# Optimization experiments

Hardware: AMD Instinct MI355X
Metric: run time of the kernel (lower is better)

Reference implementation:

```python
import jax, jax.numpy as jnp
import numpy as np

D = 256       # vec_dim
HEADS = 8     # head_num
PS = 4        # patch_size
WS = 7        # window_size (in patches)
P = WS * WS   # tokens per window


def _relative_index():
    # replicates the torch meshgrid / relative coord logic (indexing='ij')
    coords = np.stack(np.meshgrid(np.arange(WS), np.arange(WS), indexing='ij'))  # [2,WS,WS]
    cf = coords.reshape(2, -1)                                                   # [2,P]
    rc = (cf[:, :, None] - cf[:, None, :]).transpose(1, 2, 0)                    # [P,P,2]
    rc[:, :, 0] += WS - 1
    rc[:, :, 1] += WS - 1
    rc[:, :, 1] *= 2 * WS - 1
    return rc.sum(-1)  # [P,P] ints in [0,(2WS-1)^2)


def _shift_mask(ch, cw):
    # standard swin shift mask built on the patch grid (ch, cw)
    fm = np.zeros((ch, cw))
    idx = (slice(0, -WS), slice(-WS, -(WS // 2)), slice(-(WS // 2), None))
    cnt = 0
    for y in idx:
        for x in idx:
            fm[y, x] = cnt
            cnt += 1
    nh, nw = ch // WS, cw // WS
    fm = fm.reshape(nh, WS, nw, WS).transpose(0, 2, 1, 3).reshape(nh * nw, P)
    m = fm[:, None, :] - fm[:, :, None]
    return np.where(m != 0, -100.0, 0.0).astype(np.float32)


def setup_inputs() -> dict:
    key = jax.random.key(0)
    ks = jax.random.split(key, 10)
    N, PN = 8, 3136
    s = 0.02
    return {
        'inputs': jax.random.normal(ks[0], (N, D, PN), jnp.float32),
        'Wk': jax.random.normal(ks[1], (HEADS * D, D), jnp.float32) * s,
        'bk': jax.random.normal(ks[2], (HEADS * D,), jnp.float32) * s,
        'Wq': jax.random.normal(ks[3], (HEADS * D, D), jnp.float32) * s,
        'bq': jax.random.normal(ks[4], (HEADS * D,), jnp.float32) * s,
        'Wv': jax.random.normal(ks[5], (HEADS * D, D), jnp.float32) * s,
        'bv': jax.random.normal(ks[6], (HEADS * D,), jnp.float32) * s,
        'Wo': jax.random.normal(ks[7], (D, HEADS * D), jnp.float32) * s,
        'bo': jax.random.normal(ks[8], (D,), jnp.float32) * s,
        'rel_code': jax.random.normal(ks[9], ((2 * WS - 1) ** 2, HEADS), jnp.float32) * 0.02,
        'h': 224,
        'w': 224,
    }


def _forward(inputs, Wk, bk, Wq, bq, Wv, bv, Wo, bo, rel_code, h, w):
    ch, cw = h // PS, w // PS            # patch grid
    N, _, PN = inputs.shape
    C = D // (PS * PS)
    nh, nw = ch // WS, cw // WS
    WIN = nh * nw

    # patches2features -> pixel-space roll by WS//2 -> features2patches
    x = inputs.reshape(N, C, PS, PS, ch, cw)
    x = x.transpose(0, 1, 4, 2, 5, 3).reshape(N, C, ch * PS, cw * PS)
    x = jnp.roll(x, (WS // 2, WS // 2), axis=(-2, -1))
    x = x.reshape(N, C, ch, PS, cw, PS).transpose(0, 2, 4, 1, 3, 5).reshape(N, PN, D)
    x = x.transpose(0, 2, 1)  # [N,D,PN]

    def proj(W, b):
        e = jnp.einsum('od,ndp->nop', W, x) + b[None, :, None]  # [N,HEADS*D,PN]
        e = e.reshape(N, HEADS, D, ch, cw)
        # window partition: n h d (nh w1)(nw w2) -> n h (nh nw) d (w1 w2)
        e = e.reshape(N, HEADS, D, nh, WS, nw, WS)
        return e.transpose(0, 1, 3, 5, 2, 4, 6).reshape(N, HEADS, WIN, D, P)

    k = proj(Wk, bk)
    q = proj(Wq, bq)
    v = proj(Wv, bv)

    # attn[p,q] = k_p . q_q  (softmax over keys p, axis=3)
    attn = jnp.einsum('nhgdp,nhgdq->nhgpq', k, q) / (D ** 0.5)
    mask = jnp.asarray(_shift_mask(ch, cw))
    attn = attn + mask[None, None]
    rel_idx = _relative_index().ravel()
    rel = rel_code[rel_idx].reshape(P, P, HEADS).transpose(2, 0, 1)  # [H,P,P]
    attn = attn + rel[None, :, None]
    wmap = jax.nn.softmax(attn, axis=3)

    out = jnp.einsum('nhgdp,nhgpq->nhgdq', v, wmap)
    # window merge back to [N,H,D,PN]
    out = out.reshape(N, HEADS, nh, nw, D, WS, WS)
    out = out.transpose(0, 1, 4, 2, 5, 3, 6).reshape(N, HEADS * D, PN)
    return jnp.einsum('od,ndp->nop', Wo, out) + bo[None, :, None]  # [N,D,PN]


def reference(inputs, Wk, bk, Wq, bq, Wv, bv, Wo, bo, rel_code, h, w):
    return _forward(inputs, Wk, bk, Wq, bq, Wv, bv, Wo, bo, rel_code, h, w)
```

## Files before the change

kernel.cpp:

```cpp
#include <hip/hip_runtime.h>
#include <hip/hip_bf16.h>


#define NBATCH 8
#define MSTR   2176
#define TROWS  3200

typedef unsigned short ushort_t;
typedef __attribute__((ext_vector_type(8))) short bf16x8;
typedef __attribute__((ext_vector_type(8))) unsigned short u16x8;
typedef __attribute__((ext_vector_type(4))) float f32x4;

__device__ __forceinline__ float b2f(ushort_t u) {
  union { unsigned int i; float f; } v; v.i = ((unsigned int)u) << 16; return v.f;
}
__device__ __forceinline__ ushort_t f2b(float f) {
  union { float f; unsigned int u; } v; v.f = f;
  unsigned int u = v.u;
  return (ushort_t)((u + 0x7FFFu + ((u >> 16) & 1u)) >> 16);
}
__device__ __forceinline__ int regof(int y) { return (y < 49) ? 0 : ((y < 53) ? 1 : 2); }
__device__ __forceinline__ int div7(int t) { return (t * 37) >> 8; }
__device__ __forceinline__ int tmap(int p, int gi, int gj) {
  int wi = div7(p); return (gi * 7 + wi) * 56 + gj * 7 + (p - wi * 7);
}
__device__ __forceinline__ ushort4 pack4(f32x4 a) {
  ushort4 u; u.x = f2b(a[0]); u.y = f2b(a[1]); u.z = f2b(a[2]); u.w = f2b(a[3]);
  return u;
}
__device__ __forceinline__ void gload_lds16(const ushort_t* g, ushort_t* l) {
  __builtin_amdgcn_global_load_lds(
      (const __attribute__((address_space(1))) void*)g,
      (__attribute__((address_space(3))) void*)l, 16, 0, 0);
}
__device__ __forceinline__ void sb0() { __builtin_amdgcn_sched_barrier(0); }

__global__ void k_prep(const float* __restrict__ Wk, const float* __restrict__ Wq,
                       const float* __restrict__ Wo, const float* __restrict__ Wv,
                       const float* __restrict__ bk, const float* __restrict__ bq,
                       const float* __restrict__ bv, const float* __restrict__ bo,
                       const float* __restrict__ relc,
                       ushort_t* __restrict__ Aext, ushort_t* __restrict__ Wov3,
                       float* __restrict__ cvec, float* __restrict__ relL2) {
  __shared__ float red[8];
  int blk = blockIdx.x, t = threadIdx.x;
  if (blk < 512) {
    int h = blk >> 6, b0 = (blk & 63) << 2, a = t;
    const float* wkh = Wk + h * 65536;
    const float* wqh = Wq + h * 65536;
    float a0 = 0.f, a1 = 0.f, a2 = 0.f, a3 = 0.f;
    for (int dd = 0; dd < 256; ++dd) {
      float wk = wkh[dd * 256 + a];
      float4 w4 = *(const float4*)(wqh + dd * 256 + b0);
      a0 += wk * w4.x; a1 += wk * w4.y; a2 += wk * w4.z; a3 += wk * w4.w;
    }
    ushort4 u; u.x = f2b(a0); u.y = f2b(a1); u.z = f2b(a2); u.w = f2b(a3);
    *(ushort4*)(Aext + (h * 256 + a) * 256 + b0) = u;
  } else if (blk < 1024) {
    int bb = blk - 512;
    int h = bb >> 6, o0 = (bb & 63) << 2, d = t;
    float a0 = 0.f, a1 = 0.f, a2 = 0.f, a3 = 0.f;
    for (int dd = 0; dd < 256; ++dd) {
      float wv = Wv[(h * 256 + dd) * 256 + d];
      a0 += Wo[(o0 + 0) * 2048 + h * 256 + dd] * wv;
      a1 += Wo[(o0 + 1) * 2048 + h * 256 + dd] * wv;
      a2 += Wo[(o0 + 2) * 2048 + h * 256 + dd] * wv;
      a3 += Wo[(o0 + 3) * 2048 + h * 256 + dd] * wv;
    }
    Wov3[(o0 + 0) * 2048 + h * 256 + d] = f2b(a0);
    Wov3[(o0 + 1) * 2048 + h * 256 + d] = f2b(a1);
    Wov3[(o0 + 2) * 2048 + h * 256 + d] = f2b(a2);
    Wov3[(o0 + 3) * 2048 + h * 256 + d] = f2b(a3);
  } else if (blk < 1032) {
    int h = blk - 1024;
    float s1 = 0.f, s2 = 0.f;
    for (int dd = 0; dd < 256; ++dd) {
      s1 += bk[h * 256 + dd] * Wq[(h * 256 + dd) * 256 + t];
      s2 += bq[h * 256 + dd] * Wk[(h * 256 + dd) * 256 + t];
    }
    Aext[(2048 + h) * 256 + t] = f2b(s1);
    Aext[(2056 + h) * 256 + t] = f2b(s2);
  } else if (blk == 1032) {
    for (int i = t; i < 112 * 256 / 8; i += 256)
      *(u16x8*)(Aext + 2064 * 256 + i * 8) = (u16x8){0,0,0,0,0,0,0,0};
  } else if (blk < 1289) {
    int o = blk - 1033;
    const float* wob = Wo + o * 2048;
    float acc = 0.f;
#pragma unroll
    for (int j = 0; j < 8; ++j) acc += wob[j * 256 + t] * bv[j * 256 + t];
#pragma unroll
    for (int s = 1; s < 64; s <<= 1) acc += __shfl_xor(acc, s);
    if ((t & 63) == 0) red[t >> 6] = acc;
    __syncthreads();
    if (t == 0) cvec[o] = bo[o] + red[0] + red[1] + red[2] + red[3];
  } else {
    if (t < 8) {
      float c = 0.f;
      for (int dd = 0; dd < 256; ++dd) c += bk[t * 256 + dd] * bq[t * 256 + dd];
      red[t] = c * 0.0625f;
    }
    __syncthreads();
    for (int i = t; i < 8 * 169; i += 256) {
      int h = i / 169, idx = i - h * 169;
      relL2[i] = relc[idx * 8 + h] + red[h];
    }
  }
}

__global__ void k_conv(const float* __restrict__ X, ushort_t* __restrict__ Xroll) {
  const int n = blockIdx.x / 57, y = blockIdx.x % 57;
  ushort_t* xr = Xroll + (size_t)n * TROWS * 256;
  const int d = threadIdx.x;
  if (y == 56) {
    for (int i = d; i < 64 * 256 / 8; i += 256)
      *(u16x8*)(xr + 3136 * 256 + i * 8) = (u16x8){0,0,0,0,0,0,0,0};
    return;
  }
  const int c = d >> 4, p1 = (d >> 2) & 3, p2 = d & 3;
  const int sp = c * 16 + (((p1 + 1) & 3) << 2) + ((p2 + 1) & 3);
  const int ty = (p1 == 3) ? y : ((y == 0) ? 55 : y - 1);
  const float* rowp = X + (size_t)n * 256 * 3136 + sp * 3136 + ty * 56;
  ushort_t* orow = xr + y * 56 * 256 + d;
  for (int x = 0; x < 56; ++x) {
    int tx = (p2 == 3) ? x : ((x == 0) ? 55 : x - 1);
    orow[x * 256] = f2b(rowp[tx]);
  }
}

__global__ __launch_bounds__(256, 2) void k_gemm1(
    const ushort_t* __restrict__ Xroll, const ushort_t* __restrict__ Aext,
    ushort_t* __restrict__ MT) {
  const int bx0 = blockIdx.x;
  const int n = bx0 & 7;
  const int inner = bx0 >> 3;
  const int aa = inner % 17;
  const int c  = inner / 17;
  const int a0 = aa * 128;
  const int tstart = (c == 0) ? 0 : (7 * c + 1);
  const int T = (c == 0) ? 8 : 7;
  const int tid = threadIdx.x, wave = tid >> 6, lane = tid & 63;
  const int quad = lane >> 4, l16 = lane & 15;
  const int wa = wave >> 1, wt = wave & 1;
  const ushort_t* Xn = Xroll + (size_t)n * TROWS * 256;
  ushort_t* Mn = MT + (size_t)n * TROWS * MSTR;

  const ushort_t* abase = Aext + (size_t)(a0 + wa * 64 + l16) * 256 + quad * 8;
  bf16x8 areg[8][4];
#pragma unroll
  for (int kk = 0; kk < 8; ++kk)
#pragma unroll
    for (int i = 0; i < 4; ++i)
      areg[kk][i] = *(const bf16x8*)(abase + i * 4096 + kk * 32);
  sb0();

  const ushort_t* bbase =
      Xn + (size_t)(tstart * 64 + wt * 32 + l16) * 256 + quad * 8;

  for (int m = 0; m < T; ++m) {
    const ushort_t* bsrc = bbase + (size_t)m * 64 * 256;
    bf16x8 breg[8][2];
#pragma unroll
    for (int kk = 0; kk < 8; ++kk)
#pragma unroll
      for (int j = 0; j < 2; ++j)
        breg[kk][j] = *(const bf16x8*)(bsrc + j * 16 * 256 + kk * 32);
    sb0();

    f32x4 acc[4][2];
#pragma unroll
    for (int i = 0; i < 4; ++i)
#pragma unroll
      for (int j = 0; j < 2; ++j) acc[i][j] = (f32x4){0.f, 0.f, 0.f, 0.f};
#pragma unroll
    for (int kk = 0; kk < 8; ++kk)
#pragma unroll
      for (int i = 0; i < 4; ++i)
#pragma unroll
        for (int j = 0; j < 2; ++j)
          acc[i][j] = __builtin_amdgcn_mfma_f32_16x16x32_bf16(areg[kk][i], breg[kk][j], acc[i][j], 0, 0, 0);

    const int tb = (tstart + m) * 64;
#pragma unroll
    for (int i = 0; i < 4; ++i)
#pragma unroll
      for (int j = 0; j < 2; ++j) {
        int tg = tb + wt * 32 + j * 16 + l16;
        int ag = a0 + wa * 64 + i * 16 + quad * 4;
        *(ushort4*)(Mn + (size_t)tg * MSTR + ag) = pack4(acc[i][j]);
      }
  }
}

#define XP_STR 264
__global__ __launch_bounds__(512, 4) void k_attn2(
    const ushort_t* __restrict__ Xroll, ushort_t* __restrict__ MT,
    const float* __restrict__ relL2) {
  __shared__ ushort_t Xp[64 * XP_STR];
  __shared__ ushort_t StB[2][64 * 72];
  __shared__ float aqsL[8 * 64];
  __shared__ float bpsL[8 * 64];
  __shared__ float relLh[8 * 169];

  const int tid = threadIdx.x;
  const int wave = tid >> 6, lane = tid & 63;
  const int quad = lane >> 4, l16 = lane & 15;
  const int group = wave >> 2, wv = wave & 3;
  const int n = blockIdx.x >> 6, g = blockIdx.x & 63;
  const int gi = g >> 3, gj = g & 7;
  const ushort_t* Xn = Xroll + (size_t)n * TROWS * 256;
  ushort_t* Mn = MT + (size_t)n * TROWS * MSTR;

  {
    const int p = tid & 63, cg = tid >> 6;
    if (p < 49) {
      int t = tmap(p, gi, gj);
#pragma unroll
      for (int i = 0; i < 4; ++i)
        *(u16x8*)(&Xp[p * XP_STR + (cg * 4 + i) * 8]) =
            *(const u16x8*)(Xn + t * 256 + (cg * 4 + i) * 8);
    } else {
#pragma unroll
      for (int i = 0; i < 4; ++i)
        *(u16x8*)(&Xp[p * XP_STR + (cg * 4 + i) * 8]) = (u16x8){0,0,0,0,0,0,0,0};
    }
  }
  for (int i = tid; i < 8 * 169; i += 512) relLh[i] = relL2[i];
  {
    const int h = tid >> 6, q = tid & 63;
    int qq = (q < 49) ? q : 48;
    int t = tmap(qq, gi, gj);
    aqsL[h * 64 + q] = b2f(Mn[(size_t)t * MSTR + 2048 + h]);
    bpsL[h * 64 + q] = b2f(Mn[(size_t)t * MSTR + 2056 + h]);
  }
  __syncthreads();

  bf16x8 xfr[4][2];
#pragma unroll
  for (int dt = 0; dt < 4; ++dt) {
    const int d = (wv * 4 + dt) * 16 + l16;
#pragma unroll
    for (int kk = 0; kk < 2; ++kk)
#pragma unroll
      for (int j = 0; j < 8; ++j)
        xfr[dt][kk][j] = (short)Xp[(kk * 32 + quad * 8 + j) * XP_STR + d];
  }

  const int q = wv * 16 + l16;
  const int qq = (q < 49) ? q : 48;
  const int tq = tmap(qq, gi, gj);
  const ushort_t* Mbase = Mn + (size_t)tq * MSTR + quad * 8;
  const int yq = div7(qq), xq = qq - yq * 7;
  const int fq = regof(gi * 7 + yq) * 3 + regof(gj * 7 + xq);

  for (int hh = 0; hh < 4; ++hh) {
    const int h = hh * 2 + group;
    f32x4 sacc[4];
#pragma unroll
    for (int pt = 0; pt < 4; ++pt) sacc[pt] = (f32x4){0.f, 0.f, 0.f, 0.f};
    const ushort_t* mrow = Mbase + h * 256;
#pragma unroll
    for (int kk = 0; kk < 8; ++kk) {
      bf16x8 bfm = *(const bf16x8*)(mrow + kk * 32);
#pragma unroll
      for (int pt = 0; pt < 4; ++pt) {
        bf16x8 af = *(const bf16x8*)(&Xp[(pt * 16 + l16) * XP_STR + kk * 32 + quad * 8]);
        sacc[pt] = __builtin_amdgcn_mfma_f32_16x16x32_bf16(af, bfm, sacc[pt], 0, 0, 0);
      }
    }
    float v[16];
    const float aqv = aqsL[h * 64 + q];
    const float* rel_h = &relLh[h * 169];
    float m = -1e30f;
#pragma unroll
    for (int pt = 0; pt < 4; ++pt)
#pragma unroll
      for (int r = 0; r < 4; ++r) {
        int p = pt * 16 + quad * 4 + r;
        float val = -1e30f;
        if (p < 49) {
          int yp = div7(p), xp = p - yp * 7;
          int fp = regof(gi * 7 + yp) * 3 + regof(gj * 7 + xp);
          val = (sacc[pt][r] + aqv + bpsL[h * 64 + p]) * 0.0625f +
                rel_h[(yp - yq + 6) + 13 * (xp - xq + 6)];
          if (fp != fq) val -= 100.f;
        }
        v[pt * 4 + r] = val;
        m = fmaxf(m, val);
      }
    m = fmaxf(m, __shfl_xor(m, 16));
    m = fmaxf(m, __shfl_xor(m, 32));
    float s = 0.f;
#pragma unroll
    for (int i = 0; i < 16; ++i) { v[i] = __expf(v[i] - m); s += v[i]; }
    s += __shfl_xor(s, 16);
    s += __shfl_xor(s, 32);
    const float inv = 1.f / s;
    __syncthreads();
    {
      ushort_t* sb = &StB[group][q * 72];
#pragma unroll
      for (int pt = 0; pt < 4; ++pt) {
        ushort4 u;
        u.x = f2b(v[pt * 4 + 0] * inv); u.y = f2b(v[pt * 4 + 1] * inv);
        u.z = f2b(v[pt * 4 + 2] * inv); u.w = f2b(v[pt * 4 + 3] * inv);
        *(ushort4*)(&sb[pt * 16 + quad * 4]) = u;
      }
    }
    __syncthreads();
#pragma unroll
    for (int qt = 0; qt < 4; ++qt) {
      f32x4 tacc[4];
#pragma unroll
      for (int dt = 0; dt < 4; ++dt) tacc[dt] = (f32x4){0.f, 0.f, 0.f, 0.f};
#pragma unroll
      for (int kk = 0; kk < 2; ++kk) {
        bf16x8 bfw = *(const bf16x8*)(&StB[group][(qt * 16 + l16) * 72 + kk * 32 + quad * 8]);
#pragma unroll
        for (int dt = 0; dt < 4; ++dt)
          tacc[dt] = __builtin_amdgcn_mfma_f32_16x16x32_bf16(xfr[dt][kk], bfw, tacc[dt], 0, 0, 0);
      }
      int q2 = qt * 16 + l16;
      if (q2 < 49) {
        int t2 = tmap(q2, gi, gj);
#pragma unroll
        for (int dt = 0; dt < 4; ++dt) {
          int d0 = (wv * 4 + dt) * 16 + quad * 4;
          *(ushort4*)(Mn + (size_t)t2 * MSTR + h * 256 + d0) = pack4(tacc[dt]);
        }
      }
    }
  }
}

__global__ __launch_bounds__(256, 2) void k_gemm3(
    const ushort_t* __restrict__ Wov3, const ushort_t* __restrict__ MT,
    const float* __restrict__ cvec, float* __restrict__ out) {
  __shared__ ushort_t Asm[128 * 128];
  __shared__ ushort_t Bsm[128 * 128];
  const int bx0 = blockIdx.x;
  const int bx = (bx0 & 7) * 50 + (bx0 >> 3);
  const int n = bx / 50, r2 = bx % 50;
  const int oi = r2 / 25, tt = r2 % 25;
  const int o0 = oi * 128, t0 = tt * 128;
  const int tid = threadIdx.x, wave = tid >> 6, lane = tid & 63;
  const int quad = lane >> 4, l16 = lane & 15;
  const int wa = wave >> 1, wt = wave & 1;
  const ushort_t* Tn = MT + (size_t)n * TROWS * MSTR;
  float* on = out + (size_t)n * 256 * 3136;
  const int sw = l16 & 7;

  f32x4 acc[4][4];
#pragma unroll
  for (int i = 0; i < 4; ++i)
#pragma unroll
    for (int j = 0; j < 4; ++j) acc[i][j] = (f32x4){0.f, 0.f, 0.f, 0.f};

  for (int kit = 0; kit < 16; ++kit) {
    const int kb = kit * 128;
#pragma unroll
    for (int i = 0; i < 8; ++i) {
      int S = i * 256 + tid;
      int rr = S >> 4, sc = S & 15;
      int c = (sc & 8) | ((sc ^ rr) & 7);
      gload_lds16(Wov3 + (o0 + rr) * 2048 + kb + c * 8,
                  &Asm[(i * 256 + wave * 64) * 8]);
    }
#pragma unroll
    for (int i = 0; i < 8; ++i) {
      int S = i * 256 + tid;
      int rr = S >> 4, sc = S & 15;
      int c = (sc & 8) | ((sc ^ rr) & 7);
      gload_lds16(Tn + (size_t)(t0 + rr) * MSTR + kb + c * 8,
                  &Bsm[(i * 256 + wave * 64) * 8]);
    }
    __syncthreads();
#pragma unroll
    for (int kk = 0; kk < 4; ++kk) {
      bf16x8 af[4], bf[4];
      const int c = kk * 4 + quad;
      const int pos = (c & 8) | ((c ^ sw) & 7);
#pragma unroll
      for (int i = 0; i < 4; ++i)
        af[i] = *(const bf16x8*)(&Asm[(wa * 64 + i * 16 + l16) * 128 + pos * 8]);
#pragma unroll
      for (int j = 0; j < 4; ++j)
        bf[j] = *(const bf16x8*)(&Bsm[(wt * 64 + j * 16 + l16) * 128 + pos * 8]);
#pragma unroll
      for (int i = 0; i < 4; ++i)
#pragma unroll
        for (int j = 0; j < 4; ++j)
          acc[i][j] = __builtin_amdgcn_mfma_f32_16x16x32_bf16(af[i], bf[j], acc[i][j], 0, 0, 0);
    }
    __syncthreads();
  }
#pragma unroll
  for (int i = 0; i < 4; ++i) {
    const int ob = o0 + wa * 64 + i * 16 + quad * 4;
    const float4 cv = *(const float4*)(cvec + ob);
#pragma unroll
    for (int j = 0; j < 4; ++j) {
      const int tg = t0 + wt * 64 + j * 16 + l16;
      if (tg < 3136) {
        on[(size_t)(ob + 0) * 3136 + tg] = acc[i][j][0] + cv.x;
        on[(size_t)(ob + 1) * 3136 + tg] = acc[i][j][1] + cv.y;
        on[(size_t)(ob + 2) * 3136 + tg] = acc[i][j][2] + cv.z;
        on[(size_t)(ob + 3) * 3136 + tg] = acc[i][j][3] + cv.w;
      }
    }
  }
}

extern "C" void kernel_launch(void* const* d_in, const int* in_sizes, int n_in,
                              void* d_out, int out_size, void* d_ws, size_t ws_size,
                              hipStream_t stream) {
  (void)in_sizes; (void)n_in; (void)out_size; (void)ws_size;
  const float* X  = (const float*)d_in[0];
  const float* Wk = (const float*)d_in[1];
  const float* bk = (const float*)d_in[2];
  const float* Wq = (const float*)d_in[3];
  const float* bq = (const float*)d_in[4];
  const float* Wv = (const float*)d_in[5];
  const float* bv = (const float*)d_in[6];
  const float* Wo = (const float*)d_in[7];
  const float* bo = (const float*)d_in[8];
  const float* rc = (const float*)d_in[9];

  ushort_t* MT    = (ushort_t*)d_ws;
  ushort_t* Xroll = MT + (size_t)8 * TROWS * MSTR;
  ushort_t* Aext  = Xroll + (size_t)8 * TROWS * 256;
  ushort_t* Wov3  = Aext + 2176 * 256;
  float* fbase = (float*)(Wov3 + 256 * 2048);
  float* cvec  = fbase;
  float* relL2 = fbase + 256;
  float* out = (float*)d_out;

  k_prep <<<dim3(1290), dim3(256), 0, stream>>>(Wk, Wq, Wo, Wv, bk, bq, bv, bo, rc,
                                                Aext, Wov3, cvec, relL2);
  k_conv <<<dim3(8 * 57), dim3(256), 0, stream>>>(X, Xroll);
  k_gemm1<<<dim3(8 * 119), dim3(256), 0, stream>>>(Xroll, Aext, MT);
  k_attn2<<<dim3(8 * 64), dim3(512), 0, stream>>>(Xroll, MT, relL2);
  k_gemm3<<<dim3(8 * 50), dim3(256), 0, stream>>>(Wov3, MT, cvec, out);
}
```

Baseline: 311.5 us.

## Fuse projection GEMM, window attention and output GEMM into one per-window kernel

Replaces the three kernels (projection GEMM, attention, output GEMM) with a single kernel launched once per window. Each block computes its window's per-head M projection into LDS, runs the softmax and attention, and accumulates the Wo projection in registers. This removes the large MT intermediate buffer and its global write/read traffic plus two launches. In exchange there are only 512 blocks at one block per CU, Aext and Wov3 weights are re-read from global by every window, the softmax is split across two wave groups with extra barriers, and the per-head loop is fully serialized.

```diff
diff --git a/kernel.cpp b/kernel.cpp
--- a/kernel.cpp
+++ b/kernel.cpp
@@ -3,8 +3,8 @@
 
 
 #define NBATCH 8
-#define MSTR   2176
 #define TROWS  3200
+#define FSTR   264
 
 typedef unsigned short ushort_t;
 typedef __attribute__((ext_vector_type(8))) short bf16x8;
@@ -28,12 +28,6 @@
   ushort4 u; u.x = f2b(a[0]); u.y = f2b(a[1]); u.z = f2b(a[2]); u.w = f2b(a[3]);
   return u;
 }
-__device__ __forceinline__ void gload_lds16(const ushort_t* g, ushort_t* l) {
-  __builtin_amdgcn_global_load_lds(
-      (const __attribute__((address_space(1))) void*)g,
-      (__attribute__((address_space(3))) void*)l, 16, 0, 0);
-}
-__device__ __forceinline__ void sb0() { __builtin_amdgcn_sched_barrier(0); }
 
 __global__ void k_prep(const float* __restrict__ Wk, const float* __restrict__ Wq,
                        const float* __restrict__ Wo, const float* __restrict__ Wv,
@@ -128,88 +122,27 @@
   }
 }
 
-__global__ __launch_bounds__(256, 2) void k_gemm1(
+__global__ __launch_bounds__(512, 1) void k_fused(
     const ushort_t* __restrict__ Xroll, const ushort_t* __restrict__ Aext,
-    ushort_t* __restrict__ MT) {
-  const int bx0 = blockIdx.x;
-  const int n = bx0 & 7;
-  const int inner = bx0 >> 3;
-  const int aa = inner % 17;
-  const int c  = inner / 17;
-  const int a0 = aa * 128;
-  const int tstart = (c == 0) ? 0 : (7 * c + 1);
-  const int T = (c == 0) ? 8 : 7;
-  const int tid = threadIdx.x, wave = tid >> 6, lane = tid & 63;
-  const int quad = lane >> 4, l16 = lane & 15;
-  const int wa = wave >> 1, wt = wave & 1;
-  const ushort_t* Xn = Xroll + (size_t)n * TROWS * 256;
-  ushort_t* Mn = MT + (size_t)n * TROWS * MSTR;
-
-  const ushort_t* abase = Aext + (size_t)(a0 + wa * 64 + l16) * 256 + quad * 8;
-  bf16x8 areg[8][4];
-#pragma unroll
-  for (int kk = 0; kk < 8; ++kk)
-#pragma unroll
-    for (int i = 0; i < 4; ++i)
-      areg[kk][i] = *(const bf16x8*)(abase + i * 4096 + kk * 32);
-  sb0();
-
-  const ushort_t* bbase =
-      Xn + (size_t)(tstart * 64 + wt * 32 + l16) * 256 + quad * 8;
-
-  for (int m = 0; m < T; ++m) {
-    const ushort_t* bsrc = bbase + (size_t)m * 64 * 256;
-    bf16x8 breg[8][2];
-#pragma unroll
-    for (int kk = 0; kk < 8; ++kk)
-#pragma unroll
-      for (int j = 0; j < 2; ++j)
-        breg[kk][j] = *(const bf16x8*)(bsrc + j * 16 * 256 + kk * 32);
-    sb0();
-
-    f32x4 acc[4][2];
-#pragma unroll
-    for (int i = 0; i < 4; ++i)
-#pragma unroll
-      for (int j = 0; j < 2; ++j) acc[i][j] = (f32x4){0.f, 0.f, 0.f, 0.f};
-#pragma unroll
-    for (int kk = 0; kk < 8; ++kk)
-#pragma unroll
-      for (int i = 0; i < 4; ++i)
-#pragma unroll
-        for (int j = 0; j < 2; ++j)
-          acc[i][j] = __builtin_amdgcn_mfma_f32_16x16x32_bf16(areg[kk][i], breg[kk][j], acc[i][j], 0, 0, 0);
-
-    const int tb = (tstart + m) * 64;
-#pragma unroll
-    for (int i = 0; i < 4; ++i)
-#pragma unroll
-      for (int j = 0; j < 2; ++j) {
-        int tg = tb + wt * 32 + j * 16 + l16;
-        int ag = a0 + wa * 64 + i * 16 + quad * 4;
-        *(ushort4*)(Mn + (size_t)tg * MSTR + ag) = pack4(acc[i][j]);
-      }
-  }
-}
-
-#define XP_STR 264
-__global__ __launch_bounds__(512, 4) void k_attn2(
-    const ushort_t* __restrict__ Xroll, ushort_t* __restrict__ MT,
-    const float* __restrict__ relL2) {
-  __shared__ ushort_t Xp[64 * XP_STR];
-  __shared__ ushort_t StB[2][64 * 72];
+    const ushort_t* __restrict__ Wov3, const float* __restrict__ cvec,
+    const float* __restrict__ relL2, float* __restrict__ out) {
+  __shared__ ushort_t Xp[64 * FSTR];
+  __shared__ ushort_t Msm[64 * FSTR];
+  __shared__ ushort_t Tsm[64 * FSTR];
+  __shared__ ushort_t StB[64 * 72];
   __shared__ float aqsL[8 * 64];
   __shared__ float bpsL[8 * 64];
   __shared__ float relLh[8 * 169];
+  __shared__ float mPart[2][64];
+  __shared__ float sPart[2][64];
 
   const int tid = threadIdx.x;
   const int wave = tid >> 6, lane = tid & 63;
   const int quad = lane >> 4, l16 = lane & 15;
-  const int group = wave >> 2, wv = wave & 3;
-  const int n = blockIdx.x >> 6, g = blockIdx.x & 63;
+  const int n = blockIdx.x & 7, g = blockIdx.x >> 3;
   const int gi = g >> 3, gj = g & 7;
   const ushort_t* Xn = Xroll + (size_t)n * TROWS * 256;
-  ushort_t* Mn = MT + (size_t)n * TROWS * MSTR;
+  float* on = out + (size_t)n * 256 * 3136;
 
   {
     const int p = tid & 63, cg = tid >> 6;
@@ -217,195 +150,203 @@
       int t = tmap(p, gi, gj);
 #pragma unroll
       for (int i = 0; i < 4; ++i)
-        *(u16x8*)(&Xp[p * XP_STR + (cg * 4 + i) * 8]) =
+        *(u16x8*)(&Xp[p * FSTR + (cg * 4 + i) * 8]) =
             *(const u16x8*)(Xn + t * 256 + (cg * 4 + i) * 8);
     } else {
 #pragma unroll
       for (int i = 0; i < 4; ++i)
-        *(u16x8*)(&Xp[p * XP_STR + (cg * 4 + i) * 8]) = (u16x8){0,0,0,0,0,0,0,0};
+        *(u16x8*)(&Xp[p * FSTR + (cg * 4 + i) * 8]) = (u16x8){0,0,0,0,0,0,0,0};
     }
   }
   for (int i = tid; i < 8 * 169; i += 512) relLh[i] = relL2[i];
-  {
-    const int h = tid >> 6, q = tid & 63;
-    int qq = (q < 49) ? q : 48;
-    int t = tmap(qq, gi, gj);
-    aqsL[h * 64 + q] = b2f(Mn[(size_t)t * MSTR + 2048 + h]);
-    bpsL[h * 64 + q] = b2f(Mn[(size_t)t * MSTR + 2056 + h]);
-  }
   __syncthreads();
 
-  bf16x8 xfr[4][2];
-#pragma unroll
-  for (int dt = 0; dt < 4; ++dt) {
-    const int d = (wv * 4 + dt) * 16 + l16;
+  bf16x8 xfr[2][2];
+#pragma unroll
+  for (int dt = 0; dt < 2; ++dt) {
+    const int d = (wave * 2 + dt) * 16 + l16;
 #pragma unroll
     for (int kk = 0; kk < 2; ++kk)
 #pragma unroll
       for (int j = 0; j < 8; ++j)
-        xfr[dt][kk][j] = (short)Xp[(kk * 32 + quad * 8 + j) * XP_STR + d];
-  }
-
-  const int q = wv * 16 + l16;
+        xfr[dt][kk][j] = (short)Xp[(kk * 32 + quad * 8 + j) * FSTR + d];
+  }
+
+  auto m_step = [&](int h) {
+    f32x4 macc[2][4];
+#pragma unroll
+    for (int i = 0; i < 2; ++i)
+#pragma unroll
+      for (int t = 0; t < 4; ++t) macc[i][t] = (f32x4){0.f, 0.f, 0.f, 0.f};
+    const ushort_t* Ah =
+        Aext + (size_t)(h * 256 + wave * 32 + l16) * 256 + quad * 8;
+#pragma unroll
+    for (int kk = 0; kk < 8; ++kk) {
+      bf16x8 ga[2];
+#pragma unroll
+      for (int i = 0; i < 2; ++i)
+        ga[i] = *(const bf16x8*)(Ah + i * 16 * 256 + kk * 32);
+#pragma unroll
+      for (int t = 0; t < 4; ++t) {
+        bf16x8 bx_ = *(const bf16x8*)(&Xp[(t * 16 + l16) * FSTR + kk * 32 + quad * 8]);
+#pragma unroll
+        for (int i = 0; i < 2; ++i)
+          macc[i][t] = __builtin_amdgcn_mfma_f32_16x16x32_bf16(ga[i], bx_, macc[i][t], 0, 0, 0);
+      }
+    }
+#pragma unroll
+    for (int i = 0; i < 2; ++i)
+#pragma unroll
+      for (int t = 0; t < 4; ++t)
+        *(ushort4*)(&Msm[(t * 16 + l16) * FSTR + wave * 32 + i * 16 + quad * 4]) =
+            pack4(macc[i][t]);
+  };
+
+  m_step(0);
+  if (wave == 0) {
+    f32x4 eacc[4];
+#pragma unroll
+    for (int t = 0; t < 4; ++t) eacc[t] = (f32x4){0.f, 0.f, 0.f, 0.f};
+    const ushort_t* Ae = Aext + (size_t)(2048 + l16) * 256 + quad * 8;
+#pragma unroll
+    for (int kk = 0; kk < 8; ++kk) {
+      bf16x8 ea = *(const bf16x8*)(Ae + kk * 32);
+#pragma unroll
+      for (int t = 0; t < 4; ++t) {
+        bf16x8 bx_ = *(const bf16x8*)(&Xp[(t * 16 + l16) * FSTR + kk * 32 + quad * 8]);
+        eacc[t] = __builtin_amdgcn_mfma_f32_16x16x32_bf16(ea, bx_, eacc[t], 0, 0, 0);
+      }
+    }
+#pragma unroll
+    for (int t = 0; t < 4; ++t) {
+      const int tok = t * 16 + l16;
+#pragma unroll
+      for (int r = 0; r < 4; ++r) {
+        const int e = quad * 4 + r;
+        if (e < 8) aqsL[e * 64 + tok] = eacc[t][r];
+        else       bpsL[(e - 8) * 64 + tok] = eacc[t][r];
+      }
+    }
+  }
+  __syncthreads();
+
+  const int wq = wave & 3, wp = wave >> 2;
+  const int q = wq * 16 + l16;
   const int qq = (q < 49) ? q : 48;
-  const int tq = tmap(qq, gi, gj);
-  const ushort_t* Mbase = Mn + (size_t)tq * MSTR + quad * 8;
   const int yq = div7(qq), xq = qq - yq * 7;
   const int fq = regof(gi * 7 + yq) * 3 + regof(gj * 7 + xq);
 
-  for (int hh = 0; hh < 4; ++hh) {
-    const int h = hh * 2 + group;
-    f32x4 sacc[4];
-#pragma unroll
-    for (int pt = 0; pt < 4; ++pt) sacc[pt] = (f32x4){0.f, 0.f, 0.f, 0.f};
-    const ushort_t* mrow = Mbase + h * 256;
+  f32x4 oacc[2][4];
+#pragma unroll
+  for (int i = 0; i < 2; ++i)
+#pragma unroll
+    for (int j = 0; j < 4; ++j) oacc[i][j] = (f32x4){0.f, 0.f, 0.f, 0.f};
+
+  for (int h = 0; h < 8; ++h) {
+    f32x4 sacc[2];
+    sacc[0] = (f32x4){0.f, 0.f, 0.f, 0.f};
+    sacc[1] = (f32x4){0.f, 0.f, 0.f, 0.f};
 #pragma unroll
     for (int kk = 0; kk < 8; ++kk) {
-      bf16x8 bfm = *(const bf16x8*)(mrow + kk * 32);
-#pragma unroll
-      for (int pt = 0; pt < 4; ++pt) {
-        bf16x8 af = *(const bf16x8*)(&Xp[(pt * 16 + l16) * XP_STR + kk * 32 + quad * 8]);
-        sacc[pt] = __builtin_amdgcn_mfma_f32_16x16x32_bf16(af, bfm, sacc[pt], 0, 0, 0);
-      }
-    }
-    float v[16];
+      bf16x8 bfm = *(const bf16x8*)(&Msm[q * FSTR + kk * 32 + quad * 8]);
+#pragma unroll
+      for (int j = 0; j < 2; ++j) {
+        bf16x8 af = *(const bf16x8*)(&Xp[((wp * 2 + j) * 16 + l16) * FSTR + kk * 32 + quad * 8]);
+        sacc[j] = __builtin_amdgcn_mfma_f32_16x16x32_bf16(af, bfm, sacc[j], 0, 0, 0);
+      }
+    }
+    float v[8];
     const float aqv = aqsL[h * 64 + q];
     const float* rel_h = &relLh[h * 169];
-    float m = -1e30f;
-#pragma unroll
-    for (int pt = 0; pt < 4; ++pt)
+    float mw = -1e30f;
+#pragma unroll
+    for (int j = 0; j < 2; ++j)
 #pragma unroll
       for (int r = 0; r < 4; ++r) {
-        int p = pt * 16 + quad * 4 + r;
+        const int p = (wp * 2 + j) * 16 + quad * 4 + r;
         float val = -1e30f;
         if (p < 49) {
-          int yp = div7(p), xp = p - yp * 7;
-          int fp = regof(gi * 7 + yp) * 3 + regof(gj * 7 + xp);
-          val = (sacc[pt][r] + aqv + bpsL[h * 64 + p]) * 0.0625f +
+          const int yp = div7(p), xp = p - yp * 7;
+          const int fp = regof(gi * 7 + yp) * 3 + regof(gj * 7 + xp);
+          val = (sacc[j][r] + aqv + bpsL[h * 64 + p]) * 0.0625f +
                 rel_h[(yp - yq + 6) + 13 * (xp - xq + 6)];
           if (fp != fq) val -= 100.f;
         }
-        v[pt * 4 + r] = val;
-        m = fmaxf(m, val);
-      }
-    m = fmaxf(m, __shfl_xor(m, 16));
-    m = fmaxf(m, __shfl_xor(m, 32));
-    float s = 0.f;
-#pragma unroll
-    for (int i = 0; i < 16; ++i) { v[i] = __expf(v[i] - m); s += v[i]; }
-    s += __shfl_xor(s, 16);
-    s += __shfl_xor(s, 32);
-    const float inv = 1.f / s;
-    __syncthreads();
-    {
-      ushort_t* sb = &StB[group][q * 72];
-#pragma unroll
-      for (int pt = 0; pt < 4; ++pt) {
-        ushort4 u;
-        u.x = f2b(v[pt * 4 + 0] * inv); u.y = f2b(v[pt * 4 + 1] * inv);
-        u.z = f2b(v[pt * 4 + 2] * inv); u.w = f2b(v[pt * 4 + 3] * inv);
-        *(ushort4*)(&sb[pt * 16 + quad * 4]) = u;
-      }
-    }
-    __syncthreads();
+        v[j * 4 + r] = val;
+        mw = fmaxf(mw, val);
+      }
+    mw = fmaxf(mw, __shfl_xor(mw, 16));
+    mw = fmaxf(mw, __shfl_xor(mw, 32));
+    if (lane < 16) mPart[wp][wq * 16 + lane] = mw;
+    __syncthreads();
+    const float mg = fmaxf(mPart[0][q], mPart[1][q]);
+    float sw = 0.f;
+#pragma unroll
+    for (int i2 = 0; i2 < 8; ++i2) { v[i2] = __expf(v[i2] - mg); sw += v[i2]; }
+    sw += __shfl_xor(sw, 16);
+    sw += __shfl_xor(sw, 32);
+    if (lane < 16) sPart[wp][wq * 16 + lane] = sw;
+    __syncthreads();
+    const float inv = 1.f / (sPart[0][q] + sPart[1][q]);
+#pragma unroll
+    for (int j = 0; j < 2; ++j) {
+      ushort4 u;
+      u.x = f2b(v[j * 4 + 0] * inv); u.y = f2b(v[j * 4 + 1] * inv);
+      u.z = f2b(v[j * 4 + 2] * inv); u.w = f2b(v[j * 4 + 3] * inv);
+      *(ushort4*)(&StB[q * 72 + (wp * 2 + j) * 16 + quad * 4]) = u;
+    }
+    if (h < 7) m_step(h + 1);
+    __syncthreads();
+    bf16x8 wfr[2][8];
+#pragma unroll
+    for (int i = 0; i < 2; ++i)
+#pragma unroll
+      for (int kk = 0; kk < 8; ++kk)
+        wfr[i][kk] = *(const bf16x8*)(Wov3 +
+            (size_t)(wave * 32 + i * 16 + l16) * 2048 + h * 256 + kk * 32 + quad * 8);
 #pragma unroll
     for (int qt = 0; qt < 4; ++qt) {
-      f32x4 tacc[4];
-#pragma unroll
-      for (int dt = 0; dt < 4; ++dt) tacc[dt] = (f32x4){0.f, 0.f, 0.f, 0.f};
+      f32x4 tacc[2];
+      tacc[0] = (f32x4){0.f, 0.f, 0.f, 0.f};
+      tacc[1] = (f32x4){0.f, 0.f, 0.f, 0.f};
 #pragma unroll
       for (int kk = 0; kk < 2; ++kk) {
-        bf16x8 bfw = *(const bf16x8*)(&StB[group][(qt * 16 + l16) * 72 + kk * 32 + quad * 8]);
-#pragma unroll
-        for (int dt = 0; dt < 4; ++dt)
+        bf16x8 bfw = *(const bf16x8*)(&StB[(qt * 16 + l16) * 72 + kk * 32 + quad * 8]);
+#pragma unroll
+        for (int dt = 0; dt < 2; ++dt)
           tacc[dt] = __builtin_amdgcn_mfma_f32_16x16x32_bf16(xfr[dt][kk], bfw, tacc[dt], 0, 0, 0);
       }
-      int q2 = qt * 16 + l16;
+#pragma unroll
+      for (int dt = 0; dt < 2; ++dt)
+        *(ushort4*)(&Tsm[(qt * 16 + l16) * FSTR + (wave * 2 + dt) * 16 + quad * 4]) =
+            pack4(tacc[dt]);
+    }
+    __syncthreads();
+#pragma unroll
+    for (int kk = 0; kk < 8; ++kk) {
+#pragma unroll
+      for (int qt = 0; qt < 4; ++qt) {
+        bf16x8 bfo = *(const bf16x8*)(&Tsm[(qt * 16 + l16) * FSTR + kk * 32 + quad * 8]);
+#pragma unroll
+        for (int i = 0; i < 2; ++i)
+          oacc[i][qt] = __builtin_amdgcn_mfma_f32_16x16x32_bf16(wfr[i][kk], bfo, oacc[i][qt], 0, 0, 0);
+      }
+    }
+    __syncthreads();
+  }
+#pragma unroll
+  for (int i = 0; i < 2; ++i) {
+    const int ob = wave * 32 + i * 16 + quad * 4;
+    const float4 cv = *(const float4*)(cvec + ob);
+#pragma unroll
+    for (int qt = 0; qt < 4; ++qt) {
+      const int q2 = qt * 16 + l16;
       if (q2 < 49) {
-        int t2 = tmap(q2, gi, gj);
-#pragma unroll
-        for (int dt = 0; dt < 4; ++dt) {
-          int d0 = (wv * 4 + dt) * 16 + quad * 4;
-          *(ushort4*)(Mn + (size_t)t2 * MSTR + h * 256 + d0) = pack4(tacc[dt]);
-        }
-      }
-    }
-  }
-}
-
-__global__ __launch_bounds__(256, 2) void k_gemm3(
-    const ushort_t* __restrict__ Wov3, const ushort_t* __restrict__ MT,
-    const float* __restrict__ cvec, float* __restrict__ out) {
-  __shared__ ushort_t Asm[128 * 128];
-  __shared__ ushort_t Bsm[128 * 128];
-  const int bx0 = blockIdx.x;
-  const int bx = (bx0 & 7) * 50 + (bx0 >> 3);
-  const int n = bx / 50, r2 = bx % 50;
-  const int oi = r2 / 25, tt = r2 % 25;
-  const int o0 = oi * 128, t0 = tt * 128;
-  const int tid = threadIdx.x, wave = tid >> 6, lane = tid & 63;
-  const int quad = lane >> 4, l16 = lane & 15;
-  const int wa = wave >> 1, wt = wave & 1;
-  const ushort_t* Tn = MT + (size_t)n * TROWS * MSTR;
-  float* on = out + (size_t)n * 256 * 3136;
-  const int sw = l16 & 7;
-
-  f32x4 acc[4][4];
-#pragma unroll
-  for (int i = 0; i < 4; ++i)
-#pragma unroll
-    for (int j = 0; j < 4; ++j) acc[i][j] = (f32x4){0.f, 0.f, 0.f, 0.f};
-
-  for (int kit = 0; kit < 16; ++kit) {
-    const int kb = kit * 128;
-#pragma unroll
-    for (int i = 0; i < 8; ++i) {
-      int S = i * 256 + tid;
-      int rr = S >> 4, sc = S & 15;
-      int c = (sc & 8) | ((sc ^ rr) & 7);
-      gload_lds16(Wov3 + (o0 + rr) * 2048 + kb + c * 8,
-                  &Asm[(i * 256 + wave * 64) * 8]);
-    }
-#pragma unroll
-    for (int i = 0; i < 8; ++i) {
-      int S = i * 256 + tid;
-      int rr = S >> 4, sc = S & 15;
-      int c = (sc & 8) | ((sc ^ rr) & 7);
-      gload_lds16(Tn + (size_t)(t0 + rr) * MSTR + kb + c * 8,
-                  &Bsm[(i * 256 + wave * 64) * 8]);
-    }
-    __syncthreads();
-#pragma unroll
-    for (int kk = 0; kk < 4; ++kk) {
-      bf16x8 af[4], bf[4];
-      const int c = kk * 4 + quad;
-      const int pos = (c & 8) | ((c ^ sw) & 7);
-#pragma unroll
-      for (int i = 0; i < 4; ++i)
-        af[i] = *(const bf16x8*)(&Asm[(wa * 64 + i * 16 + l16) * 128 + pos * 8]);
-#pragma unroll
-      for (int j = 0; j < 4; ++j)
-        bf[j] = *(const bf16x8*)(&Bsm[(wt * 64 + j * 16 + l16) * 128 + pos * 8]);
-#pragma unroll
-      for (int i = 0; i < 4; ++i)
-#pragma unroll
-        for (int j = 0; j < 4; ++j)
-          acc[i][j] = __builtin_amdgcn_mfma_f32_16x16x32_bf16(af[i], bf[j], acc[i][j], 0, 0, 0);
-    }
-    __syncthreads();
-  }
-#pragma unroll
-  for (int i = 0; i < 4; ++i) {
-    const int ob = o0 + wa * 64 + i * 16 + quad * 4;
-    const float4 cv = *(const float4*)(cvec + ob);
-#pragma unroll
-    for (int j = 0; j < 4; ++j) {
-      const int tg = t0 + wt * 64 + j * 16 + l16;
-      if (tg < 3136) {
-        on[(size_t)(ob + 0) * 3136 + tg] = acc[i][j][0] + cv.x;
-        on[(size_t)(ob + 1) * 3136 + tg] = acc[i][j][1] + cv.y;
-        on[(size_t)(ob + 2) * 3136 + tg] = acc[i][j][2] + cv.z;
-        on[(size_t)(ob + 3) * 3136 + tg] = acc[i][j][3] + cv.w;
+        const int t2 = tmap(q2, gi, gj);
+        on[(size_t)(ob + 0) * 3136 + t2] = oacc[i][qt][0] + cv.x;
+        on[(size_t)(ob + 1) * 3136 + t2] = oacc[i][qt][1] + cv.y;
+        on[(size_t)(ob + 2) * 3136 + t2] = oacc[i][qt][2] + cv.z;
+        on[(size_t)(ob + 3) * 3136 + t2] = oacc[i][qt][3] + cv.w;
       }
     }
   }
@@ -426,8 +367,7 @@
   const float* bo = (const float*)d_in[8];
   const float* rc = (const float*)d_in[9];
 
-  ushort_t* MT    = (ushort_t*)d_ws;
-  ushort_t* Xroll = MT + (size_t)8 * TROWS * MSTR;
+  ushort_t* Xroll = (ushort_t*)d_ws;
   ushort_t* Aext  = Xroll + (size_t)8 * TROWS * 256;
   ushort_t* Wov3  = Aext + 2176 * 256;
   float* fbase = (float*)(Wov3 + 256 * 2048);
@@ -438,7 +378,5 @@
   k_prep <<<dim3(1290), dim3(256), 0, stream>>>(Wk, Wq, Wo, Wv, bk, bq, bv, bo, rc,
                                                 Aext, Wov3, cvec, relL2);
   k_conv <<<dim3(8 * 57), dim3(256), 0, stream>>>(X, Xroll);
-  k_gemm1<<<dim3(8 * 119), dim3(256), 0, stream>>>(Xroll, Aext, MT);
-  k_attn2<<<dim3(8 * 64), dim3(512), 0, stream>>>(Xroll, MT, relL2);
-  k_gemm3<<<dim3(8 * 50), dim3(256), 0, stream>>>(Wov3, MT, cvec, out);
-}
+  k_fused<<<dim3(512), dim3(512), 0, stream>>>(Xroll, Aext, Wov3, cvec, relL2, out);
+}
```

Result: faster. 305.2 us (-2.0%).
